# Optimization experiments

Hardware: AMD Instinct MI355X
Metric: run time of the kernel (lower is better)

## Reference

```python
import jax, jax.numpy as jnp
import numpy as np

N, E = 50000, 800000
IN, HID, HEADS, OUT = 128, 64, 2, 32
SLOPE = 0.2  # PyG leaky_relu default


def gat_conv(x, edge_index, edge_attr, W, att_src, att_dst, W_edge, att_edge, bias,
             heads, out_ch, concat):
    n = x.shape[0]
    src, dst = edge_index[0], edge_index[1]
    # add_self_loops with fill_value='mean': self-loop attr = mean of incoming edge_attr
    ones = jnp.ones((src.shape[0],), x.dtype)
    deg = jax.ops.segment_sum(ones, dst, num_segments=n)
    loop_attr = jax.ops.segment_sum(edge_attr, dst, num_segments=n) / jnp.maximum(deg, 1.0)[:, None]
    ar = jnp.arange(n)
    src = jnp.concatenate([src, ar])
    dst = jnp.concatenate([dst, ar])
    ea = jnp.concatenate([edge_attr, loop_attr], axis=0)  # [E+N, 1]
    # linear projections
    h = (x @ W).reshape(n, heads, out_ch)                      # [N,H,C]
    a_src = jnp.sum(h * att_src, axis=-1)                      # [N,H]
    a_dst = jnp.sum(h * att_dst, axis=-1)                      # [N,H]
    e_emb = (ea @ W_edge).reshape(-1, heads, out_ch)           # [E+N,H,C]
    a_edge = jnp.sum(e_emb * att_edge, axis=-1)                # [E+N,H]
    alpha = jax.nn.leaky_relu(a_src[src] + a_dst[dst] + a_edge, SLOPE)
    # segment softmax over destination nodes
    amax = jax.ops.segment_max(alpha, dst, num_segments=n)
    amax = jnp.where(jnp.isfinite(amax), amax, 0.0)
    ex = jnp.exp(alpha - amax[dst])
    denom = jax.ops.segment_sum(ex, dst, num_segments=n)
    coef = ex / (denom[dst] + 1e-16)                           # [E+N,H]
    out = jax.ops.segment_sum(h[src] * coef[:, :, None], dst, num_segments=n)  # [N,H,C]
    out = out.reshape(n, heads * out_ch) if concat else out.mean(axis=1)
    return out + bias


def setup_inputs() -> dict:
    key = jax.random.key(0)
    ks = jax.random.split(key, 16)
    g = lambda k, shape, fan: (jax.random.normal(k, shape, jnp.float32) / np.float32(np.sqrt(fan)))
    x = jax.random.normal(ks[0], (N, IN), jnp.float32)
    edge_index = jax.random.randint(ks[1], (2, E), 0, N)
    edge_weight = jax.random.uniform(ks[2], (E, 1), jnp.float32)
    return dict(
        x=x, edge_index=edge_index, edge_weight=edge_weight,
        W1=g(ks[3], (IN, HEADS * HID), IN),
        att_src1=g(ks[4], (1, HEADS, HID), HID),
        att_dst1=g(ks[5], (1, HEADS, HID), HID),
        We1=g(ks[6], (1, HEADS * HID), 1),
        att_edge1=g(ks[7], (1, HEADS, HID), HID),
        b1=jnp.zeros((HEADS * HID,), jnp.float32),
        W2=g(ks[8], (HEADS * HID, OUT), HEADS * HID),
        att_src2=g(ks[9], (1, 1, OUT), OUT),
        att_dst2=g(ks[10], (1, 1, OUT), OUT),
        We2=g(ks[11], (1, OUT), 1),
        att_edge2=g(ks[12], (1, 1, OUT), OUT),
        b2=jnp.zeros((OUT,), jnp.float32),
    )


def reference(x, edge_index, edge_weight, W1, att_src1, att_dst1, We1, att_edge1, b1,
              W2, att_src2, att_dst2, We2, att_edge2, b2):
    h = gat_conv(x, edge_index, edge_weight, W1, att_src1, att_dst1, We1, att_edge1, b1,
                 HEADS, HID, True)
    h = jax.nn.elu(h)
    out = gat_conv(h, edge_index, edge_weight, W2, att_src2, att_dst2, We2, att_edge2, b2,
                   1, OUT, False)
    return out
```

## Files before the change

### kernel.cpp

```cpp
#include <hip/hip_runtime.h>
#include <hip/hip_bf16.h>
#include <hip/hip_fp16.h>
#include <cstddef>

#define NN 50000
#define EE 800000
#define SB  196
#define GB  782
#define ZB  1563
#define FT  4096
#define HBK 3072

typedef _Float16 half4v __attribute__((ext_vector_type(4)));
typedef _Float16 half8v __attribute__((ext_vector_type(8)));
typedef _Float16 h2v    __attribute__((ext_vector_type(2)));
typedef float    f32x4  __attribute__((ext_vector_type(4)));

__global__ void init_k(unsigned* __restrict__ dreg,
                       const float* __restrict__ We1, const float* __restrict__ attE1,
                       const float* __restrict__ We2, const float* __restrict__ attE2,
                       float* __restrict__ cE) {
    int t = threadIdx.x;
    if (blockIdx.x == ZB) {
        __shared__ float smc[128];
        if (t < 128) smc[t] = We1[t] * attE1[t];
        __syncthreads();
        for (int off = 32; off; off >>= 1) {
            if (t < 128 && (t & 63) < off) smc[t] += smc[t + off];
            __syncthreads();
        }
        if (t == 0)  cE[0] = smc[0];
        if (t == 64) cE[1] = smc[64];
        __syncthreads();
        if (t < 32) smc[t] = We2[t] * attE2[t];
        __syncthreads();
        for (int off = 16; off; off >>= 1) {
            if (t < off) smc[t] += smc[t + off];
            __syncthreads();
        }
        if (t == 0) cE[2] = smc[0];
        return;
    }
    int i = blockIdx.x * 256 + t;
    if (i < 8 * NN) dreg[i] = 0u;
}

__global__ __launch_bounds__(256) void histgemm_k(
        const int* __restrict__ ei, unsigned* __restrict__ dreg, int* __restrict__ rank,
        const float* __restrict__ x, const float* __restrict__ W,
        const float* __restrict__ attS, const float* __restrict__ attD,
        __half* __restrict__ h1, float* __restrict__ asrc, float* __restrict__ adst) {
    __shared__ __align__(16) _Float16 xs[64 * 136];
    int t = threadIdx.x;
    int b = blockIdx.x;
    if ((b & 3) != 3) {
        int hb = (b >> 2) * 3 + (b & 3);
        for (int e = hb * 256 + t; e < EE; e += HBK * 256) {
            int dst = ei[EE + e];
            int rep = (e >> 8) & 7;
            rank[e] = (int)atomicAdd(&dreg[rep * NN + dst], 1u);
        }
        return;
    }
    int tile = b >> 2;
    if (tile >= GB) return;
    int rowbase = tile * 64;
    int wid = t >> 6, lane = t & 63;
    #pragma unroll
    for (int i = 0; i < 8; i++) {
        int idx = t + i * 256;
        int r = idx >> 5;
        int c4 = idx & 31;
        float4 v = make_float4(0.f, 0.f, 0.f, 0.f);
        if (rowbase + r < NN) v = ((const float4*)x)[(size_t)(rowbase + r) * 32 + c4];
        half4v hv = { (_Float16)v.x, (_Float16)v.y, (_Float16)v.z, (_Float16)v.w };
        *(half4v*)&xs[r * 136 + c4 * 4] = hv;
    }
    half8v bf[2][4];
    #pragma unroll
    for (int nt = 0; nt < 2; nt++)
        #pragma unroll
        for (int kk = 0; kk < 4; kk++) {
            int kb = kk * 32 + ((lane >> 4) << 3);
            int c = (wid << 5) + (nt << 4) + (lane & 15);
            half8v f;
            #pragma unroll
            for (int j = 0; j < 8; j++) f[j] = (_Float16)W[(kb + j) * 128 + c];
            bf[nt][kk] = f;
        }
    __syncthreads();
    int ar = lane & 15;
    int ak = (lane >> 4) << 3;
    f32x4 acc[4][2] = {};
    #pragma unroll
    for (int kk = 0; kk < 4; kk++) {
        half8v a[4];
        #pragma unroll
        for (int mt = 0; mt < 4; mt++)
            a[mt] = *(const half8v*)&xs[(mt * 16 + ar) * 136 + kk * 32 + ak];
        #pragma unroll
        for (int mt = 0; mt < 4; mt++)
            #pragma unroll
            for (int nt = 0; nt < 2; nt++)
                acc[mt][nt] = __builtin_amdgcn_mfma_f32_16x16x32_f16(
                    a[mt], bf[nt][kk], acc[mt][nt], 0, 0, 0);
    }
    __syncthreads();
    int drb = (lane >> 4) << 2;
    int dc = (wid << 5) + (lane & 15);
    #pragma unroll
    for (int mt = 0; mt < 4; mt++)
        #pragma unroll
        for (int nt = 0; nt < 2; nt++)
            #pragma unroll
            for (int r = 0; r < 4; r++)
                xs[(mt * 16 + drb + r) * 136 + dc + nt * 16] = (_Float16)acc[mt][nt][r];
    __syncthreads();
    int row = t >> 2;
    int cg = t & 3;
    int grow = rowbase + row;
    float sv = 0.f, dv = 0.f;
    #pragma unroll
    for (int k = 0; k < 4; k++) {
        int c0 = cg * 32 + k * 8;
        half8v hv = *(const half8v*)&xs[row * 136 + c0];
        if (grow < NN) *(half8v*)((_Float16*)h1 + (size_t)grow * 128 + c0) = hv;
        #pragma unroll
        for (int j = 0; j < 8; j++) {
            float f = (float)hv[j];
            sv += f * attS[c0 + j];
            dv += f * attD[c0 + j];
        }
    }
    sv += __shfl_xor(sv, 1);
    dv += __shfl_xor(dv, 1);
    if ((cg & 1) == 0 && grow < NN) {
        asrc[grow * 2 + (cg >> 1)] = sv;
        adst[grow * 2 + (cg >> 1)] = dv;
    }
}

__global__ void combine_k(const unsigned* __restrict__ dreg, int* __restrict__ deg,
                          unsigned short* __restrict__ repbase, int* __restrict__ bsum) {
    __shared__ int sm[256];
    int t = threadIdx.x, n = blockIdx.x * 256 + t;
    int d = 0;
    if (n < NN) {
        unsigned base = 0;
        #pragma unroll
        for (int r = 0; r < 8; r++) {
            unsigned c = dreg[r * NN + n];
            repbase[r * NN + n] = (unsigned short)base;
            base += c;
        }
        d = (int)base;
        deg[n] = d;
    }
    sm[t] = d;
    __syncthreads();
    for (int off = 128; off; off >>= 1) {
        if (t < off) sm[t] += sm[t + off];
        __syncthreads();
    }
    if (!t) bsum[blockIdx.x] = sm[0];
}

__global__ void scan_final_k(const int* __restrict__ deg, const int* __restrict__ bsum,
                             const unsigned short* __restrict__ repbase,
                             int* __restrict__ rowptr, int* __restrict__ rowbase8) {
    __shared__ int sm[256];
    __shared__ int boff_s;
    int t = threadIdx.x, b = blockIdx.x, i = b * 256 + t;
    int v0 = (t < b) ? bsum[t] : 0;
    sm[t] = v0;
    __syncthreads();
    for (int off = 128; off; off >>= 1) {
        if (t < off) sm[t] += sm[t + off];
        __syncthreads();
    }
    if (!t) boff_s = sm[0];
    __syncthreads();
    int v = (i < NN) ? deg[i] : 0;
    sm[t] = v;
    __syncthreads();
    for (int off = 1; off < 256; off <<= 1) {
        int a = (t >= off) ? sm[t - off] : 0;
        __syncthreads();
        sm[t] += a;
        __syncthreads();
    }
    if (i < NN) {
        int rp = boff_s + sm[t] - v;
        rowptr[i] = rp;
        #pragma unroll
        for (int r = 0; r < 8; r++)
            rowbase8[r * NN + i] = rp + (int)repbase[r * NN + i];
    }
    if (i == NN - 1) rowptr[NN] = boff_s + sm[t];
}

__global__ void scatter_k(const int* __restrict__ ei, const float* __restrict__ ew,
                          const int* __restrict__ rowbase8,
                          const int* __restrict__ rank, int2* __restrict__ csr) {
    int e = blockIdx.x * 256 + threadIdx.x;
    if (e >= EE) return;
    int src = ei[e];
    int dst = ei[EE + e];
    int rep = (e >> 8) & 7;
    int pos = rowbase8[rep * NN + dst] + rank[e];
    csr[pos] = make_int2(src, __float_as_int(ew[e]));
}

__global__ __launch_bounds__(256) void gemm2_k(const __half* __restrict__ z1,
                                               const float* __restrict__ W,
                                               const float* __restrict__ attS,
                                               const float* __restrict__ attD,
                                               __half* __restrict__ h2,
                                               float* __restrict__ asrc,
                                               float* __restrict__ adst) {
    __shared__ __align__(16) _Float16 xs[64 * 136];
    int rowbase = blockIdx.x * 64;
    int t = threadIdx.x;
    int wid = t >> 6, lane = t & 63;
    #pragma unroll
    for (int i = 0; i < 4; i++) {
        int idx = t + i * 256;
        int r = idx >> 4;
        int c16 = idx & 15;
        uint4 v = make_uint4(0, 0, 0, 0);
        if (rowbase + r < NN) v = ((const uint4*)z1)[(size_t)(rowbase + r) * 16 + c16];
        *(uint4*)&xs[r * 136 + c16 * 8] = v;
    }
    half8v bf[2][4];
    #pragma unroll
    for (int nt = 0; nt < 2; nt++)
        #pragma unroll
        for (int kk = 0; kk < 4; kk++) {
            int kb = kk * 32 + ((lane >> 4) << 3);
            int c = (nt << 4) + (lane & 15);
            half8v f;
            #pragma unroll
            for (int j = 0; j < 8; j++) f[j] = (_Float16)W[(kb + j) * 32 + c];
            bf[nt][kk] = f;
        }
    __syncthreads();
    int ar = lane & 15;
    int ak = (lane >> 4) << 3;
    f32x4 acc[2] = {};
    #pragma unroll
    for (int kk = 0; kk < 4; kk++) {
        half8v a = *(const half8v*)&xs[(wid * 16 + ar) * 136 + kk * 32 + ak];
        #pragma unroll
        for (int nt = 0; nt < 2; nt++)
            acc[nt] = __builtin_amdgcn_mfma_f32_16x16x32_f16(a, bf[nt][kk], acc[nt], 0, 0, 0);
    }
    __syncthreads();
    int drb = (lane >> 4) << 2;
    #pragma unroll
    for (int nt = 0; nt < 2; nt++)
        #pragma unroll
        for (int r = 0; r < 4; r++)
            xs[(wid * 16 + drb + r) * 40 + (nt << 4) + (lane & 15)] = (_Float16)acc[nt][r];
    __syncthreads();
    int row = t >> 2;
    int c8 = (t & 3) * 8;
    int grow = rowbase + row;
    half8v hv = *(const half8v*)&xs[row * 40 + c8];
    if (grow < NN) *(half8v*)((_Float16*)h2 + (size_t)grow * 32 + c8) = hv;
    float sv = 0.f, dv = 0.f;
    #pragma unroll
    for (int j = 0; j < 8; j++) {
        float f = (float)hv[j];
        sv += f * attS[c8 + j];
        dv += f * attD[c8 + j];
    }
    sv += __shfl_xor(sv, 1);
    dv += __shfl_xor(dv, 1);
    sv += __shfl_xor(sv, 2);
    dv += __shfl_xor(dv, 2);
    if ((t & 3) == 0 && grow < NN) { asrc[grow] = sv; adst[grow] = dv; }
}

__global__ __launch_bounds__(256) void agg1_k(const int* __restrict__ rowptr,
                       const int2* __restrict__ csr,
                       const __half* __restrict__ h1, const float* __restrict__ asrc,
                       const float* __restrict__ adst, const float* __restrict__ cE,
                       const float* __restrict__ b1, __half* __restrict__ z1) {
    __shared__ int    ssrc[4][128];
    __shared__ float2 sxx[4][128];
    __shared__ int2   spk[4][136];
    int wid = threadIdx.x >> 6;
    int n = (blockIdx.x * blockDim.x + threadIdx.x) >> 6;
    int lane = threadIdx.x & 63;
    if (n >= NN) return;
    int start = rowptr[n];
    int degn = rowptr[n + 1] - start;
    int total = degn + 1;
    float c0 = cE[0], c1 = cE[1];
    float ad0 = adst[n * 2], ad1 = adst[n * 2 + 1];
    float s0 = 0.f, s1 = 0.f, sumw = 0.f;
    for (int i = lane; i < degn; i += 64) {
        int2 sw = csr[start + i];
        int src = sw.x;
        float w = __int_as_float(sw.y);
        sumw += w;
        float2 as = *(const float2*)&asrc[src * 2];
        float e0 = as.x + ad0 + w * c0; e0 = e0 > 0.f ? e0 : 0.2f * e0;
        float e1 = as.y + ad1 + w * c1; e1 = e1 > 0.f ? e1 : 0.2f * e1;
        float x0 = __expf(e0), x1 = __expf(e1);
        s0 += x0; s1 += x1;
        if (i < 128) { ssrc[wid][i] = src; sxx[wid][i] = make_float2(x0, x1); }
    }
    for (int off = 32; off; off >>= 1) {
        s0 += __shfl_xor(s0, off);
        s1 += __shfl_xor(s1, off);
        sumw += __shfl_xor(sumw, off);
    }
    float la = sumw / fmaxf((float)degn, 1.0f);
    float2 asn = *(const float2*)&asrc[n * 2];
    float el0 = asn.x + ad0 + la * c0; el0 = el0 > 0.f ? el0 : 0.2f * el0;
    float el1 = asn.y + ad1 + la * c1; el1 = el1 > 0.f ? el1 : 0.2f * el1;
    float xl0 = __expf(el0), xl1 = __expf(el1);
    s0 += xl0; s1 += xl1;
    if (degn < 128 && lane == (degn & 63)) {
        ssrc[wid][degn] = n;
        sxx[wid][degn] = make_float2(xl0, xl1);
    }
    float inv0 = 1.0f / (s0 + 1e-16f), inv1 = 1.0f / (s1 + 1e-16f);
    int nst = min(total, 128);
    int nst8 = (nst + 7) & ~7;
    for (int i = lane; i < nst8; i += 64) {
        int2 pk;
        if (i < nst) {
            float2 xv = sxx[wid][i];
            __half2 hh = __floats2half2_rn(xv.x * inv0, xv.y * inv1);
            pk = make_int2(ssrc[wid][i], *(int*)&hh);
        } else pk = make_int2(n, 0);
        spk[wid][i] = pk;
    }
    int hsel = lane >> 5;
    unsigned psel = hsel ? 0x03020302u : 0x01000100u;
    unsigned loff = (unsigned)lane * 4u;
    const char* h1b_ = (const char*)h1;
    float acc0 = 0.f, acc1 = 0.f;
    for (int j = 0; j < nst8; j += 8) {
        h2v pa = {}, pb = {};
        #pragma unroll
        for (int u = 0; u < 8; u++) {
            int2 st = spk[wid][j + u];
            unsigned cs = __builtin_amdgcn_perm(0u, (unsigned)st.y, psel);
            unsigned hb = *(const unsigned*)(h1b_ + (((unsigned)st.x << 8) + loff));
            h2v c; __builtin_memcpy(&c, &cs, 4);
            h2v h; __builtin_memcpy(&h, &hb, 4);
            if (u & 1) pb = c * h + pb;
            else       pa = c * h + pa;
        }
        acc0 += (float)pa.x + (float)pb.x;
        acc1 += (float)pa.y + (float)pb.y;
    }
    for (int base = 128; base < total; base += 64) {
        int i = base + lane;
        float cc0 = 0.f, cc1 = 0.f; int src = n;
        if (i < total) {
            float w;
            if (i < degn) { int2 sw = csr[start + i]; src = sw.x; w = __int_as_float(sw.y); }
            else          { w = la; }
            float e0 = asrc[src * 2]     + ad0 + w * c0; e0 = e0 > 0.f ? e0 : 0.2f * e0;
            float e1 = asrc[src * 2 + 1] + ad1 + w * c1; e1 = e1 > 0.f ? e1 : 0.2f * e1;
            cc0 = __expf(e0) * inv0;
            cc1 = __expf(e1) * inv1;
        }
        int cnt = min(64, total - base);
        for (int jj = 0; jj < cnt; jj++) {
            int   s2 = __shfl(src, jj);
            float k0 = __shfl(cc0, jj);
            float k1 = __shfl(cc1, jj);
            float coef = hsel ? k1 : k0;
            float2 f = __half22float2(*(const __half2*)&h1[(size_t)s2 * 128 + 2 * lane]);
            acc0 += coef * f.x;
            acc1 += coef * f.y;
        }
    }
    float o0 = acc0 + b1[2 * lane];
    float o1 = acc1 + b1[2 * lane + 1];
    o0 = o0 > 0.f ? o0 : expm1f(o0);
    o1 = o1 > 0.f ? o1 : expm1f(o1);
    __half2 oz = __floats2half2_rn(o0, o1);
    *(__half2*)&z1[(size_t)n * 128 + 2 * lane] = oz;
}

__global__ __launch_bounds__(256) void agg2_k(const int* __restrict__ rowptr,
                       const int2* __restrict__ csr,
                       const __half* __restrict__ hh2, const float* __restrict__ asrc,
                       const float* __restrict__ adst, const float* __restrict__ cE,
                       const float* __restrict__ b2, float* __restrict__ out) {
    __shared__ float2 sxx[4][128];
    __shared__ int    ssrc[4][128];
    __shared__ int2   spk[4][136];
    int wid = threadIdx.x >> 6;
    int n = (blockIdx.x * blockDim.x + threadIdx.x) >> 6;
    int lane = threadIdx.x & 63;
    if (n >= NN) return;
    int start = rowptr[n];
    int degn = rowptr[n + 1] - start;
    int total = degn + 1;
    float c2 = cE[2];
    float aD = adst[n];
    float s = 0.f, sumw = 0.f;
    for (int i = lane; i < degn; i += 64) {
        int2 sw = csr[start + i];
        int src = sw.x;
        float w = __int_as_float(sw.y);
        sumw += w;
        float e = asrc[src] + aD + w * c2;
        e = e > 0.f ? e : 0.2f * e;
        float x = __expf(e);
        s += x;
        if (i < 128) { ssrc[wid][i] = src; sxx[wid][i] = make_float2(x, 0.f); }
    }
    for (int off = 32; off; off >>= 1) {
        s += __shfl_xor(s, off);
        sumw += __shfl_xor(sumw, off);
    }
    float la = sumw / fmaxf((float)degn, 1.0f);
    float el = asrc[n] + aD + la * c2; el = el > 0.f ? el : 0.2f * el;
    float xl = __expf(el);
    s += xl;
    if (degn < 128 && lane == (degn & 63)) {
        ssrc[wid][degn] = n;
        sxx[wid][degn] = make_float2(xl, 0.f);
    }
    float inv = 1.0f / (s + 1e-16f);
    int nst = min(total, 128);
    int nst8 = (nst + 7) & ~7;
    for (int i = lane; i < nst8; i += 64) {
        int2 pk;
        if (i < nst) {
            float cn = sxx[wid][i].x * inv;
            __half2 hc = __floats2half2_rn(cn, cn);
            pk = make_int2(ssrc[wid][i], *(int*)&hc);
        } else pk = make_int2(n, 0);
        spk[wid][i] = pk;
    }
    int g  = lane >> 4;
    int cp = lane & 15;
    const char* h2b_ = (const char*)hh2;
    unsigned coff = (unsigned)cp * 4u;
    float fa0 = 0.f, fa1 = 0.f;
    h2v pa = {}, pb = {};
    int fold = 0;
    for (int j = 0; j < nst8; j += 8) {
        int2 st0 = spk[wid][j + g];
        int2 st1 = spk[wid][j + 4 + g];
        unsigned hb0 = *(const unsigned*)(h2b_ + (((unsigned)st0.x << 6) + coff));
        unsigned hb1 = *(const unsigned*)(h2b_ + (((unsigned)st1.x << 6) + coff));
        h2v c0v; __builtin_memcpy(&c0v, &st0.y, 4);
        h2v c1v; __builtin_memcpy(&c1v, &st1.y, 4);
        h2v h0; __builtin_memcpy(&h0, &hb0, 4);
        h2v h1v; __builtin_memcpy(&h1v, &hb1, 4);
        pa = c0v * h0 + pa;
        pb = c1v * h1v + pb;
        if (++fold == 4) {
            fa0 += (float)pa.x + (float)pb.x;
            fa1 += (float)pa.y + (float)pb.y;
            pa = {}; pb = {};
            fold = 0;
        }
    }
    fa0 += (float)pa.x + (float)pb.x;
    fa1 += (float)pa.y + (float)pb.y;
    for (int i = 128; i < total; i++) {
        int src; float w;
        if (i < degn) { int2 sw = csr[start + i]; src = sw.x; w = __int_as_float(sw.y); }
        else          { src = n;                  w = la; }
        float e = asrc[src] + aD + w * c2;
        e = e > 0.f ? e : 0.2f * e;
        float cc = __expf(e) * inv;
        if (g == 0) {
            unsigned hb = *(const unsigned*)(h2b_ + (((unsigned)src << 6) + coff));
            h2v h; __builtin_memcpy(&h, &hb, 4);
            fa0 += cc * (float)h.x;
            fa1 += cc * (float)h.y;
        }
    }
    fa0 += __shfl_xor(fa0, 16); fa1 += __shfl_xor(fa1, 16);
    fa0 += __shfl_xor(fa0, 32); fa1 += __shfl_xor(fa1, 32);
    if (lane < 16) {
        float2 o = make_float2(fa0 + b2[2 * cp], fa1 + b2[2 * cp + 1]);
        *(float2*)&out[(size_t)n * 32 + 2 * cp] = o;
    }
}

extern "C" void kernel_launch(void* const* d_in, const int* in_sizes, int n_in,
                              void* d_out, int out_size, void* d_ws, size_t ws_size,
                              hipStream_t stream) {
    const float* x     = (const float*)d_in[0];
    const int*   ei    = (const int*)d_in[1];
    const float* ew    = (const float*)d_in[2];
    const float* W1    = (const float*)d_in[3];
    const float* attS1 = (const float*)d_in[4];
    const float* attD1 = (const float*)d_in[5];
    const float* We1   = (const float*)d_in[6];
    const float* attE1 = (const float*)d_in[7];
    const float* b1    = (const float*)d_in[8];
    const float* W2    = (const float*)d_in[9];
    const float* attS2 = (const float*)d_in[10];
    const float* attD2 = (const float*)d_in[11];
    const float* We2   = (const float*)d_in[12];
    const float* attE2 = (const float*)d_in[13];
    const float* b2    = (const float*)d_in[14];

    char* ws = (char*)d_ws;
    size_t off = 0;
    auto alloc = [&](size_t bytes) -> void* {
        void* p = ws + off;
        off = (off + bytes + 255) & ~(size_t)255;
        return p;
    };
    unsigned*       dreg     = (unsigned*)alloc((size_t)NN * 8 * 4);
    unsigned short* repbase  = (unsigned short*)alloc((size_t)NN * 8 * 2);
    int*            rowbase8 = (int*)alloc((size_t)NN * 8 * 4);
    int*    rank    = (int*)alloc((size_t)EE * 4);
    int*    deg     = (int*)alloc((size_t)NN * 4);
    int*    rowptr  = (int*)alloc((size_t)(NN + 1) * 4);
    int2*   csr     = (int2*)alloc((size_t)EE * 8);
    __half* h1b     = (__half*)alloc((size_t)NN * 128 * 2);
    __half* z1      = (__half*)alloc((size_t)NN * 128 * 2);
    __half* h2b     = (__half*)alloc((size_t)NN * 32 * 2);
    float*  asrc1   = (float*)alloc((size_t)NN * 2 * 4);
    float*  adst1   = (float*)alloc((size_t)NN * 2 * 4);
    float*  asrc2   = (float*)alloc((size_t)NN * 4);
    float*  adst2   = (float*)alloc((size_t)NN * 4);
    float*  cE      = (float*)alloc(4 * 4);
    int*    bsum    = (int*)alloc(256 * 4);

    const int EB  = (EE + 255) / 256;
    const int NWB = (NN * 64 + 255) / 256;

    init_k<<<ZB + 1, 256, 0, stream>>>(dreg, We1, attE1, We2, attE2, cE);
    histgemm_k<<<FT, 256, 0, stream>>>(ei, dreg, rank, x, W1, attS1, attD1,
                                       h1b, asrc1, adst1);
    combine_k<<<SB, 256, 0, stream>>>(dreg, deg, repbase, bsum);
    scan_final_k<<<SB, 256, 0, stream>>>(deg, bsum, repbase, rowptr, rowbase8);
    scatter_k<<<EB, 256, 0, stream>>>(ei, ew, rowbase8, rank, csr);

    agg1_k<<<NWB, 256, 0, stream>>>(rowptr, csr, h1b, asrc1, adst1, cE, b1, z1);
    gemm2_k<<<GB, 256, 0, stream>>>(z1, W2, attS2, attD2, h2b, asrc2, adst2);
    agg2_k<<<NWB, 256, 0, stream>>>(rowptr, csr, h2b, asrc2, adst2, cE, b2, (float*)d_out);
}
```

Before: 156.4 us.

## Fuse GEMM1 into init kernel and split histogram into its own launch

Layer-1 projection GEMM blocks move out of the histogram kernel and into the zero-init kernel. The degree histogram now runs as a separate one-edge-per-thread kernel with the replica index taken from the block index. The intent is to run the GEMM alongside the zero-fill, since neither depends on the other, and to simplify the atomic histogram. In exchange, the histogram no longer overlaps with the GEMM, and the kernel count stays the same.

Measured after the change: 141.5 us. 1.11x faster.

```diff
diff --git a/kernel.cpp b/kernel.cpp
--- a/kernel.cpp
+++ b/kernel.cpp
@@ -8,62 +8,49 @@
 #define SB  196
 #define GB  782
 #define ZB  1563
-#define FT  4096
-#define HBK 3072
 
 typedef _Float16 half4v __attribute__((ext_vector_type(4)));
 typedef _Float16 half8v __attribute__((ext_vector_type(8)));
 typedef _Float16 h2v    __attribute__((ext_vector_type(2)));
 typedef float    f32x4  __attribute__((ext_vector_type(4)));
 
-__global__ void init_k(unsigned* __restrict__ dreg,
-                       const float* __restrict__ We1, const float* __restrict__ attE1,
-                       const float* __restrict__ We2, const float* __restrict__ attE2,
-                       float* __restrict__ cE) {
-    int t = threadIdx.x;
-    if (blockIdx.x == ZB) {
-        __shared__ float smc[128];
-        if (t < 128) smc[t] = We1[t] * attE1[t];
-        __syncthreads();
-        for (int off = 32; off; off >>= 1) {
-            if (t < 128 && (t & 63) < off) smc[t] += smc[t + off];
-            __syncthreads();
-        }
-        if (t == 0)  cE[0] = smc[0];
-        if (t == 64) cE[1] = smc[64];
-        __syncthreads();
-        if (t < 32) smc[t] = We2[t] * attE2[t];
-        __syncthreads();
-        for (int off = 16; off; off >>= 1) {
-            if (t < off) smc[t] += smc[t + off];
-            __syncthreads();
-        }
-        if (t == 0) cE[2] = smc[0];
-        return;
-    }
-    int i = blockIdx.x * 256 + t;
-    if (i < 8 * NN) dreg[i] = 0u;
-}
-
-__global__ __launch_bounds__(256) void histgemm_k(
-        const int* __restrict__ ei, unsigned* __restrict__ dreg, int* __restrict__ rank,
+__global__ __launch_bounds__(256) void initgemm_k(
+        unsigned* __restrict__ dreg,
+        const float* __restrict__ We1, const float* __restrict__ attE1,
+        const float* __restrict__ We2, const float* __restrict__ attE2,
+        float* __restrict__ cE,
         const float* __restrict__ x, const float* __restrict__ W,
         const float* __restrict__ attS, const float* __restrict__ attD,
         __half* __restrict__ h1, float* __restrict__ asrc, float* __restrict__ adst) {
     __shared__ __align__(16) _Float16 xs[64 * 136];
     int t = threadIdx.x;
     int b = blockIdx.x;
-    if ((b & 3) != 3) {
-        int hb = (b >> 2) * 3 + (b & 3);
-        for (int e = hb * 256 + t; e < EE; e += HBK * 256) {
-            int dst = ei[EE + e];
-            int rep = (e >> 8) & 7;
-            rank[e] = (int)atomicAdd(&dreg[rep * NN + dst], 1u);
-        }
+    if (b < ZB) {
+        int i = b * 256 + t;
+        if (i < 8 * NN) dreg[i] = 0u;
         return;
     }
-    int tile = b >> 2;
-    if (tile >= GB) return;
+    if (b == ZB) {
+        float* smc = (float*)xs;
+        if (t < 128) smc[t] = We1[t] * attE1[t];
+        __syncthreads();
+        for (int off = 32; off; off >>= 1) {
+            if (t < 128 && (t & 63) < off) smc[t] += smc[t + off];
+            __syncthreads();
+        }
+        if (t == 0)  cE[0] = smc[0];
+        if (t == 64) cE[1] = smc[64];
+        __syncthreads();
+        if (t < 32) smc[t] = We2[t] * attE2[t];
+        __syncthreads();
+        for (int off = 16; off; off >>= 1) {
+            if (t < off) smc[t] += smc[t + off];
+            __syncthreads();
+        }
+        if (t == 0) cE[2] = smc[0];
+        return;
+    }
+    int tile = b - ZB - 1;
     int rowbase = tile * 64;
     int wid = t >> 6, lane = t & 63;
     #pragma unroll
@@ -138,6 +125,15 @@
         asrc[grow * 2 + (cg >> 1)] = sv;
         adst[grow * 2 + (cg >> 1)] = dv;
     }
+}
+
+__global__ void hist_k(const int* __restrict__ ei, unsigned* __restrict__ dreg,
+                       int* __restrict__ rank) {
+    int e = blockIdx.x * 256 + threadIdx.x;
+    if (e >= EE) return;
+    int dst = ei[EE + e];
+    int rep = blockIdx.x & 7;
+    rank[e] = (int)atomicAdd(&dreg[rep * NN + dst], 1u);
 }
 
 __global__ void combine_k(const unsigned* __restrict__ dreg, int* __restrict__ deg,
@@ -537,9 +533,9 @@
     const int EB  = (EE + 255) / 256;
     const int NWB = (NN * 64 + 255) / 256;
 
-    init_k<<<ZB + 1, 256, 0, stream>>>(dreg, We1, attE1, We2, attE2, cE);
-    histgemm_k<<<FT, 256, 0, stream>>>(ei, dreg, rank, x, W1, attS1, attD1,
-                                       h1b, asrc1, adst1);
+    initgemm_k<<<ZB + 1 + GB, 256, 0, stream>>>(dreg, We1, attE1, We2, attE2, cE,
+                                                x, W1, attS1, attD1, h1b, asrc1, adst1);
+    hist_k<<<EB, 256, 0, stream>>>(ei, dreg, rank);
     combine_k<<<SB, 256, 0, stream>>>(dreg, deg, repbase, bsum);
     scan_final_k<<<SB, 256, 0, stream>>>(deg, bsum, repbase, rowptr, rowbase8);
     scatter_k<<<EB, 256, 0, stream>>>(ei, ew, rowbase8, rank, csr);
```
